# Performance work log

Hardware: AMD Instinct MI355X
Metric: run time of the kernel (lower is better)

The kernel has to match this reference:

```python
import jax, jax.numpy as jnp
import numpy as np

N_CORES = 64
N_QUBITS = 1024
QEMB = 256
N_EDGES = 448
BATCH = 512
NN_DIMS = (256, 512, 512, 256)


def setup_inputs() -> dict:
    key = jax.random.key(0)
    ks = jax.random.split(key, 12)
    inp = {
        "core_allocs": jax.random.randint(ks[0], (BATCH, N_QUBITS), 0, N_CORES, dtype=jnp.int32),
        "qubit_embs": jax.random.normal(ks[1], (N_QUBITS, QEMB), dtype=jnp.float32),
        "dummy_qubit_emb": jax.random.normal(ks[2], (QEMB,), dtype=jnp.float32),
        "edge_index": jax.random.randint(ks[3], (2, N_EDGES), 0, N_CORES, dtype=jnp.int32),
        "edge_weight": jax.random.uniform(ks[4], (N_EDGES,), dtype=jnp.float32),
        "W1": jax.random.normal(ks[5], (NN_DIMS[0], NN_DIMS[1]), dtype=jnp.float32) * 0.05,
        "b1": jax.random.normal(ks[6], (NN_DIMS[1],), dtype=jnp.float32) * 0.05,
        "W2": jax.random.normal(ks[7], (NN_DIMS[1], NN_DIMS[2]), dtype=jnp.float32) * 0.05,
        "b2": jax.random.normal(ks[8], (NN_DIMS[2],), dtype=jnp.float32) * 0.05,
        "W3": jax.random.normal(ks[9], (NN_DIMS[2], NN_DIMS[3]), dtype=jnp.float32) * 0.05,
        "b3": jax.random.normal(ks[10], (NN_DIMS[3],), dtype=jnp.float32) * 0.05,
    }
    return inp


def _gcn_norm(edge_index, edge_weight):
    # PyG gcn_norm: add self loops (weight 1), symmetric D^{-1/2} A D^{-1/2}.
    self_idx = jnp.arange(N_CORES, dtype=edge_index.dtype)
    row = jnp.concatenate([edge_index[0], self_idx])
    col = jnp.concatenate([edge_index[1], self_idx])
    w = jnp.concatenate([edge_weight, jnp.ones((N_CORES,), edge_weight.dtype)])
    deg = jax.ops.segment_sum(w, col, num_segments=N_CORES)  # degree at targets
    dinv = jnp.where(deg > 0, deg ** -0.5, 0.0)
    norm = dinv[row] * w * dinv[col]
    return row, col, norm


def reference(core_allocs, qubit_embs, dummy_qubit_emb, edge_index, edge_weight,
              W1, b1, W2, b2, W3, b3):
    # ---- unmixedCoreEmbs, vectorized: per-core max over assigned qubit embs,
    # dummy emb always included (cores never at capacity) ----
    def pool(alloc):  # alloc: [n_qubits] -> [n_cores, qemb]
        seg = jax.ops.segment_max(qubit_embs, alloc, num_segments=N_CORES)
        return jnp.maximum(seg, dummy_qubit_emb)  # also fixes -inf empty cores

    x = jax.vmap(pool)(core_allocs)  # [B, n_cores, qemb]

    # ---- GCNConv stack (same graph replicated per batch element) ----
    row, col, norm = _gcn_norm(edge_index, edge_weight)

    def gcn_layer(h, W, b):
        hw = h @ W  # [B, C, d_out]
        msg = hw[:, row, :] * norm[None, :, None]  # gather sources, scale
        agg = jnp.zeros((h.shape[0], N_CORES, W.shape[1]), hw.dtype).at[:, col, :].add(msg)
        return jax.nn.relu(agg + b)

    x = gcn_layer(x, W1, b1)
    x = gcn_layer(x, W2, b2)
    x = gcn_layer(x, W3, b3)
    return x  # [B, n_cores, nn_dims[-1]] (original returns this split per batch element)
```

## Files before the change

### kernel.cpp

```cpp
#include <hip/hip_runtime.h>
#include <type_traits>

typedef __attribute__((ext_vector_type(8))) short short8;
typedef __attribute__((ext_vector_type(4))) short short4v;
typedef __attribute__((ext_vector_type(2))) short short2v;
typedef __attribute__((ext_vector_type(4))) float f32x4;
typedef unsigned short u16;
typedef unsigned int u32;

#define N_EDGES 448

#define WS_ADJA 0
#define WS_ADJB 4096
#define WS_W1   8192
#define WS_W2   139264
#define WS_W3   401408
#define WS_DUM  532480
#define WS_B1   (WS_DUM + 256)
#define WS_B2   (WS_DUM + 768)
#define WS_B3   (WS_DUM + 1280)
#define WS_QE   534528
#define WS_FLAG 796672

__device__ __forceinline__ float bf2f(u16 v) {
    u32 u = ((u32)v) << 16;
    return __builtin_bit_cast(float, u);
}
__device__ __forceinline__ u16 f2bf(float f) {
    u32 u = __builtin_bit_cast(u32, f);
    u32 r = u + 0x7FFFu + ((u >> 16) & 1u);
    return (u16)(r >> 16);
}
__device__ __forceinline__ u16 f2bf_fast(float f) {
    u32 u = __builtin_bit_cast(u32, f);
    return (u16)((u + 0x8000u) >> 16);
}
__device__ __forceinline__ float ldf(const void* p, int idx, u32 isf32) {
    return isf32 ? ((const float*)p)[idx] : bf2f(((const u16*)p)[idx]);
}
__device__ __forceinline__ u16 keyb(u16 b) {
    return (u16)(b ^ ((u16)(((u16)((short)b >> 15)) >> 1)));
}
__device__ __forceinline__ u32 pkmax(u32 a, u32 b) {
    short2v x = __builtin_bit_cast(short2v, a);
    short2v y = __builtin_bit_cast(short2v, b);
    short2v r = __builtin_elementwise_max(x, y);
    return __builtin_bit_cast(u32, r);
}

__global__ __launch_bounds__(512) void prep(
    const int* __restrict__ eidx, const void* __restrict__ ew,
    const void* __restrict__ qembs, const void* __restrict__ dummy,
    const void* __restrict__ W1, const void* __restrict__ b1,
    const void* __restrict__ W2, const void* __restrict__ b2,
    const void* __restrict__ W3, const void* __restrict__ b3,
    u16* __restrict__ ws) {
    const int t = threadIdx.x, bb = blockIdx.x;
    __shared__ u32 s_isf;
    if (t < 64) {
        const u16* qs = (const u16*)qembs;
        int c = 0;
#pragma unroll
        for (int j = 0; j < 4; j++) {
            u16 v = qs[(t * 4 + j) * 2];
            u32 e = (v >> 7) & 0xFF;
            c += (e >= 100 && e <= 134) ? 1 : 0;
        }
#pragma unroll
        for (int off = 32; off > 0; off >>= 1) c += __shfl_down(c, off, 64);
        if (t == 0) s_isf = (c < 128) ? 1u : 0u;
    }
    __syncthreads();
    const u32 isf32 = s_isf;

    if (t < 128) {
        const int bw = bb * 2 + (t >> 6);
        const int tl = t & 63;
        const void* src;
        int N, K32, dst, nt, kk;
        if (bw < 256)      { src = W1; N = 512; K32 = 8;  dst = WS_W1; nt = bw / 8;          kk = bw % 8; }
        else if (bw < 768) { src = W2; N = 512; K32 = 16; dst = WS_W2; nt = (bw - 256) / 16; kk = (bw - 256) % 16; }
        else               { src = W3; N = 256; K32 = 16; dst = WS_W3; nt = (bw - 768) / 16; kk = (bw - 768) % 16; }
        const int col = nt * 16 + (tl & 15);
        const int krow = kk * 32 + (tl >> 4) * 8;
        u16 v[8];
#pragma unroll
        for (int j = 0; j < 8; j++) v[j] = f2bf(ldf(src, (krow + j) * N + col, isf32));
        u16* o = ws + dst + (nt * K32 + kk) * 512 + tl * 8;
#pragma unroll
        for (int j = 0; j < 8; j++) o[j] = v[j];
    }
    if (t >= 256) {
        const int base = bb * 512 + (t - 256) * 2;
        ws[WS_QE + base]     = keyb(f2bf(ldf(qembs, base, isf32)));
        ws[WS_QE + base + 1] = keyb(f2bf(ldf(qembs, base + 1, isf32)));
    }
    if (bb == 1) {
#pragma unroll
        for (int j = 0; j < 4; j++) {
            int i = t + j * 512;
            if (i < 1792) {
                u16 o;
                if (i < 256)       o = keyb(f2bf(ldf(dummy, i, isf32)));
                else if (i < 768)  o = f2bf(ldf(b1, i - 256, isf32));
                else if (i < 1280) o = f2bf(ldf(b2, i - 768, isf32));
                else               o = f2bf(ldf(b3, i - 1280, isf32));
                ws[WS_DUM + i] = o;
            }
        }
    }
    if (bb == 0) {
        __shared__ float A[4096];
        __shared__ float deg[64];
        __shared__ float dinv[64];
        __shared__ int er[N_EDGES];
        __shared__ int ec[N_EDGES];
        __shared__ float ewf[N_EDGES];
        if (t < N_EDGES) {
            er[t] = eidx[t];
            ec[t] = eidx[N_EDGES + t];
            ewf[t] = ldf(ew, t, isf32);
        }
        if (t < 64) deg[t] = 1.0f;
        for (int i = t; i < 4096; i += 512) A[i] = 0.f;
        __syncthreads();
        if (t < N_EDGES) atomicAdd(&deg[ec[t]], ewf[t]);
        __syncthreads();
        if (t < 64) dinv[t] = 1.0f / sqrtf(deg[t]);
        __syncthreads();
        if (t < N_EDGES) atomicAdd(&A[ec[t] * 64 + er[t]], dinv[er[t]] * ewf[t] * dinv[ec[t]]);
        __syncthreads();
        if (t < 64) A[t * 64 + t] += dinv[t] * dinv[t];
        __syncthreads();
        for (int i = t; i < 4096; i += 512) {
            int chunk = i >> 9, m = (i >> 3) & 63, j = i & 7;
            ws[WS_ADJA + i] = f2bf(A[m * 64 + chunk * 8 + j]);
        }
        for (int i = t; i < 4096; i += 512) {
            int chunk = i >> 9, l = (i >> 3) & 63, j = i & 7;
            int ntc = chunk >> 1, kk = chunk & 1;
            int k = kk * 32 + (l >> 4) * 8 + j;
            int c2 = ntc * 16 + (l & 15);
            ws[WS_ADJB + i] = f2bf(A[c2 * 64 + k]);
        }
        if (t == 0) *(u32*)(ws + WS_FLAG) = isf32;
    }
}

__global__ __launch_bounds__(1024, 4) void fused(
    const int* __restrict__ allocs, const u16* __restrict__ ws,
    void* __restrict__ out) {

    __shared__ __align__(16) u16 BUF[2][64 * 512];
    __shared__ __align__(16) u16 ADJB_S[4096];

    const int t = threadIdx.x, bb = blockIdx.x;
    const int wave = t >> 6, lane = t & 63, quad = lane >> 4, nl = lane & 15;
    const u32 isf32 = *(const u32*)(ws + WS_FLAG);
    const int e0 = bb * 2;

    if (t < 512) *(uint4*)(ADJB_S + t * 8) = *(const uint4*)(ws + WS_ADJB + t * 8);

    {
        int* LISTA = (int*)(BUF[0] + 16384);
        int* CNTA  = LISTA + 1024;
        int* SSTA  = CNTA + 64;
        int* WOFA  = SSTA + 64;
        int* LISTB = (int*)(BUF[1] + 16384);
        int* CNTB  = LISTB + 1024;
        int* SSTB  = CNTB + 64;
        int* WOFB  = SSTB + 64;
        if (t < 64) { CNTA[t] = 0; CNTB[t] = 0; }
        __syncthreads();
        const int ca = allocs[e0 * 1024 + t];
        const int cb = allocs[(e0 + 1) * 1024 + t];
        atomicAdd(&CNTA[ca], 1);
        atomicAdd(&CNTB[cb], 1);
        __syncthreads();
        if (t < 128) {
            const int l = t & 63;
            int* C  = (t < 64) ? CNTA : CNTB;
            int* S  = (t < 64) ? SSTA : SSTB;
            int* Wo = (t < 64) ? WOFA : WOFB;
            int v = C[l], s = v;
#pragma unroll
            for (int off = 1; off < 64; off <<= 1) {
                int u = __shfl_up(s, off, 64);
                if (l >= off) s += u;
            }
            S[l] = s - v;
            Wo[l] = s - v;
        }
        __syncthreads();
        {
            int pa = atomicAdd(&WOFA[ca], 1); LISTA[pa] = t;
            int pb = atomicAdd(&WOFB[cb], 1); LISTB[pb] = t;
        }
        __syncthreads();
        const u16* wsq = ws + WS_QE;
        const uint2 dk = *(const uint2*)(ws + WS_DUM + lane * 4);
#pragma unroll
        for (int e = 0; e < 2; e++) {
            const int* LIST = e ? LISTB : LISTA;
            const int* CNT  = e ? CNTB  : CNTA;
            const int* SST  = e ? SSTB  : SSTA;
            u16* XB = BUF[e];
            for (int i = 0; i < 4; i++) {
                const int c = wave * 4 + i;
                const int L = CNT[c], S = SST[c];
                u32 m0 = dk.x, m1 = dk.y;
                int j = 0;
                for (; j + 4 <= L; j += 4) {
                    const int q0 = LIST[S + j],     q1 = LIST[S + j + 1];
                    const int q2 = LIST[S + j + 2], q3 = LIST[S + j + 3];
                    uint2 ra = *(const uint2*)(wsq + q0 * 256 + lane * 4);
                    uint2 rb = *(const uint2*)(wsq + q1 * 256 + lane * 4);
                    uint2 rc = *(const uint2*)(wsq + q2 * 256 + lane * 4);
                    uint2 rd = *(const uint2*)(wsq + q3 * 256 + lane * 4);
                    m0 = pkmax(pkmax(m0, ra.x), pkmax(rb.x, rc.x));
                    m1 = pkmax(pkmax(m1, ra.y), pkmax(rb.y, rc.y));
                    m0 = pkmax(m0, rd.x);
                    m1 = pkmax(m1, rd.y);
                }
                for (; j < L; j++) {
                    const int q = LIST[S + j];
                    uint2 r = *(const uint2*)(wsq + q * 256 + lane * 4);
                    m0 = pkmax(m0, r.x);
                    m1 = pkmax(m1, r.y);
                }
                short4v p;
                p[0] = (short)keyb((u16)(m0 & 0xffffu));
                p[1] = (short)keyb((u16)(m0 >> 16));
                p[2] = (short)keyb((u16)(m1 & 0xffffu));
                p[3] = (short)keyb((u16)(m1 >> 16));
                *(short4v*)(XB + (lane >> 1) * 512 + c * 8 + (lane & 1) * 4) = p;
            }
        }
    }
    __syncthreads();

    auto layerT = [&](auto K32c, const u16* __restrict__ W, const u16* __restrict__ bias) {
        constexpr int K32 = decltype(K32c)::value;
        const int s0 = wave * 2;
        f32x4 acc[2][2][4];
#pragma unroll
        for (int e = 0; e < 2; e++)
#pragma unroll
            for (int s = 0; s < 2; s++)
#pragma unroll
                for (int rt = 0; rt < 4; rt++) acc[e][s][rt] = f32x4{0.f, 0.f, 0.f, 0.f};
#pragma unroll
        for (int kk = 0; kk < K32; kk++) {
            short8 bch[2];
#pragma unroll
            for (int s = 0; s < 2; s++)
                bch[s] = *(const short8*)(W + ((s0 + s) * K32 + kk) * 512 + lane * 8);
#pragma unroll
            for (int e = 0; e < 2; e++) {
                short8 a[4];
#pragma unroll
                for (int rt = 0; rt < 4; rt++)
                    a[rt] = *(const short8*)(BUF[e] + (kk * 4 + quad) * 512 + (rt * 16 + nl) * 8);
#pragma unroll
                for (int s = 0; s < 2; s++)
#pragma unroll
                    for (int rt = 0; rt < 4; rt++)
                        acc[e][s][rt] = __builtin_amdgcn_mfma_f32_16x16x32_bf16(a[rt], bch[s], acc[e][s][rt], 0, 0, 0);
            }
        }
        __syncthreads();
#pragma unroll
        for (int s = 0; s < 2; s++) {
            const int nt = s0 + s;
            float bv[4];
#pragma unroll
            for (int rr = 0; rr < 4; rr++) bv[rr] = bf2f(bias[nt * 16 + quad * 4 + rr]);
#pragma unroll
            for (int e = 0; e < 2; e++) {
                u16* scr = BUF[e] + (wave * 4 + 2) * 512;
                f32x4 agg[4];
#pragma unroll
                for (int ntc = 0; ntc < 4; ntc++) agg[ntc] = f32x4{0.f, 0.f, 0.f, 0.f};
#pragma unroll
                for (int h = 0; h < 2; h++) {
#pragma unroll
                    for (int r2 = 0; r2 < 2; r2++) {
                        f32x4 v = acc[e][s][2 * h + r2];
                        short4v p;
#pragma unroll
                        for (int rr = 0; rr < 4; rr++) p[rr] = (short)f2bf_fast(v[rr]);
                        *(short4v*)(scr + nl * 40 + r2 * 16 + quad * 4) = p;
                    }
                    short8 hwf = *(const short8*)(scr + nl * 40 + quad * 8);
#pragma unroll
                    for (int ntc = 0; ntc < 4; ntc++) {
                        short8 bfrag = *(const short8*)(ADJB_S + (ntc * 2 + h) * 512 + lane * 8);
                        agg[ntc] = __builtin_amdgcn_mfma_f32_16x16x32_bf16(hwf, bfrag, agg[ntc], 0, 0, 0);
                    }
                }
#pragma unroll
                for (int ntc = 0; ntc < 4; ntc++) {
                    short4v p;
#pragma unroll
                    for (int rr = 0; rr < 4; rr++)
                        p[rr] = (short)f2bf_fast(fmaxf(agg[ntc][rr] + bv[rr], 0.f));
                    *(short4v*)(BUF[e] + (nt * 2 + (quad >> 1)) * 512 + (ntc * 16 + nl) * 8 + (quad & 1) * 4) = p;
                }
            }
        }
        __syncthreads();
    };

    auto layer3 = [&](const u16* __restrict__ W) {
        const int nt = wave;
        f32x4 acc[2][4];
#pragma unroll
        for (int e = 0; e < 2; e++)
#pragma unroll
            for (int rt = 0; rt < 4; rt++) acc[e][rt] = f32x4{0.f, 0.f, 0.f, 0.f};
#pragma unroll
        for (int kk = 0; kk < 16; kk++) {
            short8 bch = *(const short8*)(W + (nt * 16 + kk) * 512 + lane * 8);
#pragma unroll
            for (int e = 0; e < 2; e++) {
                short8 a[4];
#pragma unroll
                for (int rt = 0; rt < 4; rt++)
                    a[rt] = *(const short8*)(BUF[e] + (kk * 4 + quad) * 512 + (rt * 16 + nl) * 8);
#pragma unroll
                for (int rt = 0; rt < 4; rt++)
                    acc[e][rt] = __builtin_amdgcn_mfma_f32_16x16x32_bf16(a[rt], bch, acc[e][rt], 0, 0, 0);
            }
        }
        __syncthreads();
#pragma unroll
        for (int e = 0; e < 2; e++) {
            u16* scr = BUF[e] + 16384 + wave * 640;
#pragma unroll
            for (int h = 0; h < 2; h++) {
#pragma unroll
                for (int r2 = 0; r2 < 2; r2++) {
                    f32x4 v = acc[e][2 * h + r2];
                    short4v p;
#pragma unroll
                    for (int rr = 0; rr < 4; rr++) p[rr] = (short)f2bf_fast(v[rr]);
                    *(short4v*)(scr + nl * 40 + r2 * 16 + quad * 4) = p;
                }
                short8 hwf = *(const short8*)(scr + nl * 40 + quad * 8);
                *(short8*)(BUF[e] + (nt * 2 + h) * 512 + lane * 8) = hwf;
            }
        }
        __syncthreads();
    };

    layerT(std::integral_constant<int, 8>{},  ws + WS_W1, ws + WS_B1);
    layerT(std::integral_constant<int, 16>{}, ws + WS_W2, ws + WS_B2);
    layer3(ws + WS_W3);

    {
        const int rt2 = wave & 3, nt0 = (wave >> 2) * 4;
        short8 aA[2];
#pragma unroll
        for (int h = 0; h < 2; h++)
            aA[h] = *(const short8*)(ws + WS_ADJA + (h * 4 + quad) * 512 + (rt2 * 16 + nl) * 8);
        f32x4 accv[2][4];
#pragma unroll
        for (int e = 0; e < 2; e++)
#pragma unroll
            for (int ni = 0; ni < 4; ni++) {
                const int nt = nt0 + ni;
                short8 b0v = *(const short8*)(BUF[e] + (nt * 2 + 0) * 512 + lane * 8);
                short8 b1v = *(const short8*)(BUF[e] + (nt * 2 + 1) * 512 + lane * 8);
                f32x4 a = f32x4{0.f, 0.f, 0.f, 0.f};
                a = __builtin_amdgcn_mfma_f32_16x16x32_bf16(aA[0], b0v, a, 0, 0, 0);
                a = __builtin_amdgcn_mfma_f32_16x16x32_bf16(aA[1], b1v, a, 0, 0, 0);
                accv[e][ni] = a;
            }
        __syncthreads();
#pragma unroll
        for (int e = 0; e < 2; e++) {
            float* Hf = (float*)BUF[e];
#pragma unroll
            for (int ni = 0; ni < 4; ni++) {
                const int n = (nt0 + ni) * 16 + nl;
                const float bv = bf2f(ws[WS_B3 + n]);
#pragma unroll
                for (int rr = 0; rr < 4; rr++) {
                    const int m2 = rt2 * 16 + quad * 4 + rr;
                    Hf[m2 * 256 + n] = fmaxf(accv[e][ni][rr] + bv, 0.f);
                }
            }
        }
        __syncthreads();
        if (isf32) {
#pragma unroll
            for (int e = 0; e < 2; e++) {
                float4* outv = (float4*)((float*)out + (size_t)(e0 + e) * 16384);
                const float4* Hv = (const float4*)(BUF[e]);
#pragma unroll
                for (int p4 = 0; p4 < 4; p4++) outv[p4 * 1024 + t] = Hv[p4 * 1024 + t];
            }
        } else {
#pragma unroll
            for (int e = 0; e < 2; e++) {
                u16* outu = (u16*)out + (size_t)(e0 + e) * 16384;
                const float* Hf = (const float*)BUF[e];
#pragma unroll
                for (int p4 = 0; p4 < 4; p4++) {
                    const int idx = (p4 * 1024 + t) * 4;
                    float4 v = *(const float4*)(Hf + idx);
                    short4v pk;
                    pk[0] = (short)f2bf_fast(v.x); pk[1] = (short)f2bf_fast(v.y);
                    pk[2] = (short)f2bf_fast(v.z); pk[3] = (short)f2bf_fast(v.w);
                    *(short4v*)(outu + idx) = pk;
                }
            }
        }
    }
}

extern "C" void kernel_launch(void* const* d_in, const int* in_sizes, int n_in,
                              void* d_out, int out_size, void* d_ws, size_t ws_size,
                              hipStream_t stream) {
    const int* allocs = (const int*)d_in[0];
    const void* qembs = d_in[1];
    const void* dummy = d_in[2];
    const int* eidx   = (const int*)d_in[3];
    const void* ew    = d_in[4];
    const void* W1 = d_in[5];
    const void* b1 = d_in[6];
    const void* W2 = d_in[7];
    const void* b2 = d_in[8];
    const void* W3 = d_in[9];
    const void* b3 = d_in[10];
    u16* ws = (u16*)d_ws;

    prep<<<512, 512, 0, stream>>>(eidx, ew, qembs, dummy, W1, b1, W2, b2, W3, b3, ws);
    fused<<<256, 1024, 0, stream>>>(allocs, ws, d_out);
}
```

Baseline: 141.2 us.

## Split block's waves across the two batch elements instead of interleaving both

Each block of 16 waves now assigns waves 0-7 to batch element A and waves 8-15 to element B, instead of every wave handling both elements. Each wave now covers twice as many output column tiles of one element, so A fragments loaded from LDS are reused across four weight columns instead of two. The aim is to halve the LDS A-fragment traffic per MFMA. The cost is twice as many global weight fragment loads per wave and different register pressure under the 1024-thread launch bound.

```diff
diff --git a/kernel.cpp b/kernel.cpp
--- a/kernel.cpp
+++ b/kernel.cpp
@@ -156,6 +156,8 @@
 
     const int t = threadIdx.x, bb = blockIdx.x;
     const int wave = t >> 6, lane = t & 63, quad = lane >> 4, nl = lane & 15;
+    const int he = wave >> 3;
+    const int w8 = wave & 7;
     const u32 isf32 = *(const u32*)(ws + WS_FLAG);
     const int e0 = bb * 2;
 
@@ -199,155 +201,144 @@
         __syncthreads();
         const u16* wsq = ws + WS_QE;
         const uint2 dk = *(const uint2*)(ws + WS_DUM + lane * 4);
-#pragma unroll
-        for (int e = 0; e < 2; e++) {
-            const int* LIST = e ? LISTB : LISTA;
-            const int* CNT  = e ? CNTB  : CNTA;
-            const int* SST  = e ? SSTB  : SSTA;
-            u16* XB = BUF[e];
-            for (int i = 0; i < 4; i++) {
-                const int c = wave * 4 + i;
-                const int L = CNT[c], S = SST[c];
-                u32 m0 = dk.x, m1 = dk.y;
-                int j = 0;
-                for (; j + 4 <= L; j += 4) {
-                    const int q0 = LIST[S + j],     q1 = LIST[S + j + 1];
-                    const int q2 = LIST[S + j + 2], q3 = LIST[S + j + 3];
-                    uint2 ra = *(const uint2*)(wsq + q0 * 256 + lane * 4);
-                    uint2 rb = *(const uint2*)(wsq + q1 * 256 + lane * 4);
-                    uint2 rc = *(const uint2*)(wsq + q2 * 256 + lane * 4);
-                    uint2 rd = *(const uint2*)(wsq + q3 * 256 + lane * 4);
-                    m0 = pkmax(pkmax(m0, ra.x), pkmax(rb.x, rc.x));
-                    m1 = pkmax(pkmax(m1, ra.y), pkmax(rb.y, rc.y));
-                    m0 = pkmax(m0, rd.x);
-                    m1 = pkmax(m1, rd.y);
-                }
-                for (; j < L; j++) {
-                    const int q = LIST[S + j];
-                    uint2 r = *(const uint2*)(wsq + q * 256 + lane * 4);
-                    m0 = pkmax(m0, r.x);
-                    m1 = pkmax(m1, r.y);
-                }
-                short4v p;
-                p[0] = (short)keyb((u16)(m0 & 0xffffu));
-                p[1] = (short)keyb((u16)(m0 >> 16));
-                p[2] = (short)keyb((u16)(m1 & 0xffffu));
-                p[3] = (short)keyb((u16)(m1 >> 16));
-                *(short4v*)(XB + (lane >> 1) * 512 + c * 8 + (lane & 1) * 4) = p;
-            }
+        const int* LIST = he ? LISTB : LISTA;
+        const int* CNT  = he ? CNTB  : CNTA;
+        const int* SST  = he ? SSTB  : SSTA;
+        u16* XB = BUF[he];
+        for (int i = 0; i < 8; i++) {
+            const int c = w8 * 8 + i;
+            const int L = CNT[c], S = SST[c];
+            u32 m0 = dk.x, m1 = dk.y;
+            int j = 0;
+            for (; j + 4 <= L; j += 4) {
+                const int q0 = LIST[S + j],     q1 = LIST[S + j + 1];
+                const int q2 = LIST[S + j + 2], q3 = LIST[S + j + 3];
+                uint2 ra = *(const uint2*)(wsq + q0 * 256 + lane * 4);
+                uint2 rb = *(const uint2*)(wsq + q1 * 256 + lane * 4);
+                uint2 rc = *(const uint2*)(wsq + q2 * 256 + lane * 4);
+                uint2 rd = *(const uint2*)(wsq + q3 * 256 + lane * 4);
+                m0 = pkmax(pkmax(m0, ra.x), pkmax(rb.x, rc.x));
+                m1 = pkmax(pkmax(m1, ra.y), pkmax(rb.y, rc.y));
+                m0 = pkmax(m0, rd.x);
+                m1 = pkmax(m1, rd.y);
+            }
+            for (; j < L; j++) {
+                const int q = LIST[S + j];
+                uint2 r = *(const uint2*)(wsq + q * 256 + lane * 4);
+                m0 = pkmax(m0, r.x);
+                m1 = pkmax(m1, r.y);
+            }
+            short4v p;
+            p[0] = (short)keyb((u16)(m0 & 0xffffu));
+            p[1] = (short)keyb((u16)(m0 >> 16));
+            p[2] = (short)keyb((u16)(m1 & 0xffffu));
+            p[3] = (short)keyb((u16)(m1 >> 16));
+            *(short4v*)(XB + (lane >> 1) * 512 + c * 8 + (lane & 1) * 4) = p;
         }
     }
     __syncthreads();
 
     auto layerT = [&](auto K32c, const u16* __restrict__ W, const u16* __restrict__ bias) {
         constexpr int K32 = decltype(K32c)::value;
-        const int s0 = wave * 2;
-        f32x4 acc[2][2][4];
-#pragma unroll
-        for (int e = 0; e < 2; e++)
-#pragma unroll
-            for (int s = 0; s < 2; s++)
-#pragma unroll
-                for (int rt = 0; rt < 4; rt++) acc[e][s][rt] = f32x4{0.f, 0.f, 0.f, 0.f};
+        const int s0 = w8 * 4;
+        u16* scr = BUF[he] + (w8 * 8 + 6) * 512;
+        f32x4 acc[4][4];
+#pragma unroll
+        for (int s = 0; s < 4; s++)
+#pragma unroll
+            for (int rt = 0; rt < 4; rt++) acc[s][rt] = f32x4{0.f, 0.f, 0.f, 0.f};
 #pragma unroll
         for (int kk = 0; kk < K32; kk++) {
-            short8 bch[2];
-#pragma unroll
-            for (int s = 0; s < 2; s++)
+            short8 a[4], bch[4];
+#pragma unroll
+            for (int rt = 0; rt < 4; rt++)
+                a[rt] = *(const short8*)(BUF[he] + (kk * 4 + quad) * 512 + (rt * 16 + nl) * 8);
+#pragma unroll
+            for (int s = 0; s < 4; s++)
                 bch[s] = *(const short8*)(W + ((s0 + s) * K32 + kk) * 512 + lane * 8);
 #pragma unroll
-            for (int e = 0; e < 2; e++) {
-                short8 a[4];
+            for (int s = 0; s < 4; s++)
 #pragma unroll
                 for (int rt = 0; rt < 4; rt++)
-                    a[rt] = *(const short8*)(BUF[e] + (kk * 4 + quad) * 512 + (rt * 16 + nl) * 8);
-#pragma unroll
-                for (int s = 0; s < 2; s++)
-#pragma unroll
-                    for (int rt = 0; rt < 4; rt++)
-                        acc[e][s][rt] = __builtin_amdgcn_mfma_f32_16x16x32_bf16(a[rt], bch[s], acc[e][s][rt], 0, 0, 0);
-            }
-        }
-        __syncthreads();
-#pragma unroll
-        for (int s = 0; s < 2; s++) {
+                    acc[s][rt] = __builtin_amdgcn_mfma_f32_16x16x32_bf16(a[rt], bch[s], acc[s][rt], 0, 0, 0);
+        }
+        __syncthreads();
+#pragma unroll
+        for (int s = 0; s < 4; s++) {
             const int nt = s0 + s;
             float bv[4];
 #pragma unroll
             for (int rr = 0; rr < 4; rr++) bv[rr] = bf2f(bias[nt * 16 + quad * 4 + rr]);
-#pragma unroll
-            for (int e = 0; e < 2; e++) {
-                u16* scr = BUF[e] + (wave * 4 + 2) * 512;
-                f32x4 agg[4];
-#pragma unroll
-                for (int ntc = 0; ntc < 4; ntc++) agg[ntc] = f32x4{0.f, 0.f, 0.f, 0.f};
-#pragma unroll
-                for (int h = 0; h < 2; h++) {
-#pragma unroll
-                    for (int r2 = 0; r2 < 2; r2++) {
-                        f32x4 v = acc[e][s][2 * h + r2];
-                        short4v p;
-#pragma unroll
-                        for (int rr = 0; rr < 4; rr++) p[rr] = (short)f2bf_fast(v[rr]);
-                        *(short4v*)(scr + nl * 40 + r2 * 16 + quad * 4) = p;
-                    }
-                    short8 hwf = *(const short8*)(scr + nl * 40 + quad * 8);
-#pragma unroll
-                    for (int ntc = 0; ntc < 4; ntc++) {
-                        short8 bfrag = *(const short8*)(ADJB_S + (ntc * 2 + h) * 512 + lane * 8);
-                        agg[ntc] = __builtin_amdgcn_mfma_f32_16x16x32_bf16(hwf, bfrag, agg[ntc], 0, 0, 0);
-                    }
-                }
-#pragma unroll
-                for (int ntc = 0; ntc < 4; ntc++) {
-                    short4v p;
-#pragma unroll
-                    for (int rr = 0; rr < 4; rr++)
-                        p[rr] = (short)f2bf_fast(fmaxf(agg[ntc][rr] + bv[rr], 0.f));
-                    *(short4v*)(BUF[e] + (nt * 2 + (quad >> 1)) * 512 + (ntc * 16 + nl) * 8 + (quad & 1) * 4) = p;
-                }
-            }
-        }
-        __syncthreads();
-    };
-
-    auto layer3 = [&](const u16* __restrict__ W) {
-        const int nt = wave;
-        f32x4 acc[2][4];
-#pragma unroll
-        for (int e = 0; e < 2; e++)
-#pragma unroll
-            for (int rt = 0; rt < 4; rt++) acc[e][rt] = f32x4{0.f, 0.f, 0.f, 0.f};
-#pragma unroll
-        for (int kk = 0; kk < 16; kk++) {
-            short8 bch = *(const short8*)(W + (nt * 16 + kk) * 512 + lane * 8);
-#pragma unroll
-            for (int e = 0; e < 2; e++) {
-                short8 a[4];
-#pragma unroll
-                for (int rt = 0; rt < 4; rt++)
-                    a[rt] = *(const short8*)(BUF[e] + (kk * 4 + quad) * 512 + (rt * 16 + nl) * 8);
-#pragma unroll
-                for (int rt = 0; rt < 4; rt++)
-                    acc[e][rt] = __builtin_amdgcn_mfma_f32_16x16x32_bf16(a[rt], bch, acc[e][rt], 0, 0, 0);
-            }
-        }
-        __syncthreads();
-#pragma unroll
-        for (int e = 0; e < 2; e++) {
-            u16* scr = BUF[e] + 16384 + wave * 640;
+            f32x4 agg[4];
+#pragma unroll
+            for (int ntc = 0; ntc < 4; ntc++) agg[ntc] = f32x4{0.f, 0.f, 0.f, 0.f};
 #pragma unroll
             for (int h = 0; h < 2; h++) {
 #pragma unroll
                 for (int r2 = 0; r2 < 2; r2++) {
-                    f32x4 v = acc[e][2 * h + r2];
+                    f32x4 v = acc[s][2 * h + r2];
                     short4v p;
 #pragma unroll
                     for (int rr = 0; rr < 4; rr++) p[rr] = (short)f2bf_fast(v[rr]);
                     *(short4v*)(scr + nl * 40 + r2 * 16 + quad * 4) = p;
                 }
                 short8 hwf = *(const short8*)(scr + nl * 40 + quad * 8);
-                *(short8*)(BUF[e] + (nt * 2 + h) * 512 + lane * 8) = hwf;
+#pragma unroll
+                for (int ntc = 0; ntc < 4; ntc++) {
+                    short8 bfrag = *(const short8*)(ADJB_S + (ntc * 2 + h) * 512 + lane * 8);
+                    agg[ntc] = __builtin_amdgcn_mfma_f32_16x16x32_bf16(hwf, bfrag, agg[ntc], 0, 0, 0);
+                }
+            }
+#pragma unroll
+            for (int ntc = 0; ntc < 4; ntc++) {
+                short4v p;
+#pragma unroll
+                for (int rr = 0; rr < 4; rr++)
+                    p[rr] = (short)f2bf_fast(fmaxf(agg[ntc][rr] + bv[rr], 0.f));
+                *(short4v*)(BUF[he] + (nt * 2 + (quad >> 1)) * 512 + (ntc * 16 + nl) * 8 + (quad & 1) * 4) = p;
+            }
+        }
+        __syncthreads();
+    };
+
+    auto layer3 = [&](const u16* __restrict__ W) {
+        f32x4 acc[2][4];
+#pragma unroll
+        for (int s = 0; s < 2; s++)
+#pragma unroll
+            for (int rt = 0; rt < 4; rt++) acc[s][rt] = f32x4{0.f, 0.f, 0.f, 0.f};
+#pragma unroll
+        for (int kk = 0; kk < 16; kk++) {
+            short8 a[4], bch[2];
+#pragma unroll
+            for (int rt = 0; rt < 4; rt++)
+                a[rt] = *(const short8*)(BUF[he] + (kk * 4 + quad) * 512 + (rt * 16 + nl) * 8);
+#pragma unroll
+            for (int s = 0; s < 2; s++)
+                bch[s] = *(const short8*)(W + ((w8 * 2 + s) * 16 + kk) * 512 + lane * 8);
+#pragma unroll
+            for (int s = 0; s < 2; s++)
+#pragma unroll
+                for (int rt = 0; rt < 4; rt++)
+                    acc[s][rt] = __builtin_amdgcn_mfma_f32_16x16x32_bf16(a[rt], bch[s], acc[s][rt], 0, 0, 0);
+        }
+        __syncthreads();
+        u16* scr = BUF[he] + 16384 + w8 * 640;
+#pragma unroll
+        for (int s = 0; s < 2; s++) {
+            const int nt = w8 * 2 + s;
+#pragma unroll
+            for (int h = 0; h < 2; h++) {
+#pragma unroll
+                for (int r2 = 0; r2 < 2; r2++) {
+                    f32x4 v = acc[s][2 * h + r2];
+                    short4v p;
+#pragma unroll
+                    for (int rr = 0; rr < 4; rr++) p[rr] = (short)f2bf_fast(v[rr]);
+                    *(short4v*)(scr + nl * 40 + r2 * 16 + quad * 4) = p;
+                }
+                short8 hwf = *(const short8*)(scr + nl * 40 + quad * 8);
+                *(short8*)(BUF[he] + (nt * 2 + h) * 512 + lane * 8) = hwf;
             }
         }
         __syncthreads();
@@ -358,36 +349,33 @@
     layer3(ws + WS_W3);
 
     {
-        const int rt2 = wave & 3, nt0 = (wave >> 2) * 4;
+        const int rt2 = w8 & 3, nt0 = (w8 >> 2) * 8;
         short8 aA[2];
 #pragma unroll
         for (int h = 0; h < 2; h++)
             aA[h] = *(const short8*)(ws + WS_ADJA + (h * 4 + quad) * 512 + (rt2 * 16 + nl) * 8);
-        f32x4 accv[2][4];
-#pragma unroll
-        for (int e = 0; e < 2; e++)
-#pragma unroll
-            for (int ni = 0; ni < 4; ni++) {
-                const int nt = nt0 + ni;
-                short8 b0v = *(const short8*)(BUF[e] + (nt * 2 + 0) * 512 + lane * 8);
-                short8 b1v = *(const short8*)(BUF[e] + (nt * 2 + 1) * 512 + lane * 8);
-                f32x4 a = f32x4{0.f, 0.f, 0.f, 0.f};
-                a = __builtin_amdgcn_mfma_f32_16x16x32_bf16(aA[0], b0v, a, 0, 0, 0);
-                a = __builtin_amdgcn_mfma_f32_16x16x32_bf16(aA[1], b1v, a, 0, 0, 0);
-                accv[e][ni] = a;
-            }
-        __syncthreads();
-#pragma unroll
-        for (int e = 0; e < 2; e++) {
-            float* Hf = (float*)BUF[e];
-#pragma unroll
-            for (int ni = 0; ni < 4; ni++) {
+        f32x4 accv[8];
+#pragma unroll
+        for (int ni = 0; ni < 8; ni++) {
+            const int nt = nt0 + ni;
+            short8 b0v = *(const short8*)(BUF[he] + (nt * 2 + 0) * 512 + lane * 8);
+            short8 b1v = *(const short8*)(BUF[he] + (nt * 2 + 1) * 512 + lane * 8);
+            f32x4 a = f32x4{0.f, 0.f, 0.f, 0.f};
+            a = __builtin_amdgcn_mfma_f32_16x16x32_bf16(aA[0], b0v, a, 0, 0, 0);
+            a = __builtin_amdgcn_mfma_f32_16x16x32_bf16(aA[1], b1v, a, 0, 0, 0);
+            accv[ni] = a;
+        }
+        __syncthreads();
+        {
+            float* Hf = (float*)BUF[he];
+#pragma unroll
+            for (int ni = 0; ni < 8; ni++) {
                 const int n = (nt0 + ni) * 16 + nl;
                 const float bv = bf2f(ws[WS_B3 + n]);
 #pragma unroll
                 for (int rr = 0; rr < 4; rr++) {
                     const int m2 = rt2 * 16 + quad * 4 + rr;
-                    Hf[m2 * 256 + n] = fmaxf(accv[e][ni][rr] + bv, 0.f);
+                    Hf[m2 * 256 + n] = fmaxf(accv[ni][rr] + bv, 0.f);
                 }
             }
         }
```

Result: slower. 159.0 us (+12.6%).
